# Kernel tuning notes

Measured on AMD Instinct MI355X. Metric: run time of the kernel, lower is better.

The kernel has to match this reference:

```python
import jax, jax.numpy as jnp
import numpy as np

H = 768        # hidden_size (rubert-base)
WDIM = 30      # width_embedding_dim (SpanRepresentation default)
MAXW = 10      # max_span_width
HID = 150      # PairwiseScorer hidden_dim
LN_EPS = 1e-5


def setup_inputs() -> dict:
    key = jax.random.key(0)
    ks = jax.random.split(key, 12)
    B, S, N = 4, 2048, 4096
    p = lambda i, shape: jax.random.normal(ks[i], shape, dtype=jnp.float32) * 0.02
    return {
        "sequence_output": jax.random.normal(ks[0], (B, S, H), dtype=jnp.float32),
        "span_starts": jax.random.randint(ks[1], (B, N), 0, S),
        "span_ends": jax.random.randint(ks[2], (B, N), 0, S),
        "W_start": p(3, (H, H)), "b_start": jnp.zeros((H,), jnp.float32),
        "W_end": p(4, (H, H)), "b_end": jnp.zeros((H,), jnp.float32),
        "width_emb": p(5, (MAXW + 1, WDIM)),
        "W_out": p(6, (2 * H + WDIM, H)), "b_out": jnp.zeros((H,), jnp.float32),
        "w_ment": p(7, (H,)), "b_ment": jnp.zeros((), jnp.float32),
        "W1": p(8, (4 * H, HID)), "b1": jnp.zeros((HID,), jnp.float32),
        "ln_g": jnp.ones((HID,), jnp.float32), "ln_b": jnp.zeros((HID,), jnp.float32),
        "W2": p(9, (HID,)), "b2": jnp.zeros((), jnp.float32),
        "top_k": 128,
    }


def reference(sequence_output, span_starts, span_ends,
              W_start, b_start, W_end, b_end, width_emb, W_out, b_out,
              w_ment, b_ment, W1, b1, ln_g, ln_b, W2, b2, top_k):
    # --- SpanRepresentation: gather endpoints, endpoint FFs, width embedding ---
    st = jnp.take_along_axis(sequence_output, span_starts[..., None], axis=1)  # [B,N,H]
    en = jnp.take_along_axis(sequence_output, span_ends[..., None], axis=1)    # [B,N,H]
    start_e = st @ W_start + b_start
    end_e = en @ W_end + b_end
    widths = jnp.clip(span_ends - span_starts, 0, MAXW)
    we = width_emb[widths]                                                     # [B,N,WDIM]
    span_repr = jnp.concatenate([start_e, end_e, we], axis=-1) @ W_out + b_out # [B,N,H]

    # --- MentionScorer + top-k filtering (per batch, vectorized) ---
    scores = span_repr @ w_ment + b_ment                                       # [B,N]
    mention_scores, idx = jax.lax.top_k(scores, top_k)                         # [B,K]
    repr_k = jnp.take_along_axis(span_repr, idx[..., None], axis=1)            # [B,K,H]
    f_starts = jnp.take_along_axis(span_starts, idx, axis=1)
    f_ends = jnp.take_along_axis(span_ends, idx, axis=1)

    # --- PairwiseScorer over all pairs: cat([s1,s2,s1-s2,s1*s2]) @ W1 ---
    # Split W1 rows into the four feature blocks; fold the (s1-s2) block in:
    #   z = s1@(Wa+Wc) + s2@(Wb-Wc) + (s1*s2)@Wd + b1
    Wa, Wb, Wc, Wd = W1[:H], W1[H:2*H], W1[2*H:3*H], W1[3*H:]
    u = repr_k @ (Wa + Wc)                                                     # [B,K,HID]
    v = repr_k @ (Wb - Wc)                                                     # [B,K,HID]
    pw = jnp.einsum('bih,bjh,hd->bijd', repr_k, repr_k, Wd)                    # [B,K,K,HID]
    z = u[:, :, None, :] + v[:, None, :, :] + pw + b1
    h = jax.nn.relu(z)
    mu = jnp.mean(h, axis=-1, keepdims=True)
    var = jnp.mean(jnp.square(h - mu), axis=-1, keepdims=True)
    hn = (h - mu) * jax.lax.rsqrt(var + LN_EPS) * ln_g + ln_b
    # Dropout(0.3) is identity in eval mode.
    ant = hn @ W2 + b2                                                         # [B,K,K]
    ant = jnp.tril(ant, k=-1)

    return (mention_scores, ant, f_starts, f_ends)
```

## Files before the change

### kernel.cpp

```cpp
#include <hip/hip_runtime.h>
#include <math.h>

#define H 768
#define SEQ 2048
#define NSP 4096
#define HIDD 150
#define TOPK 128
#define NPAD 160

#define OFS_ANT 512
#define OFS_FS 66048
#define OFS_FE 66560

static const size_t OFF_T     = 0ull;
static const size_t OFF_BIASP = 8448ull;
static const size_t OFF_WOV   = 14592ull;
static const size_t OFF_AV    = 16128ull;
static const size_t OFF_CV    = 16896ull;
static const size_t OFF_TW    = 17664ull;
static const size_t OFF_PD    = 17680ull;
static const size_t OFF_CAND  = 34064ull;
static const size_t OFF_FS    = 42256ull;
static const size_t OFF_FE    = 42768ull;
static const size_t OFF_WID   = 43280ull;
static const size_t OFF_UVP   = 43792ull;
static const size_t OFF_GW    = 371472ull;
static const size_t OFF_SCAL  = 371632ull;
static const size_t OFF_WF    = 371640ull;
static const size_t OFF_WCF   = 433080ull;
static const size_t OFF_WSF   = 555960ull;
static const size_t OFF_WEF   = 850872ull;
static const size_t OFF_WOF   = 1145784ull;
static const size_t OFF_SEH   = 1735608ull;
static const size_t OFF_RKH   = 2128824ull;
static const size_t OFF_RKP2  = 2325432ull;

typedef __attribute__((ext_vector_type(8))) _Float16 half8;
typedef __attribute__((ext_vector_type(4))) _Float16 half4;
typedef __attribute__((ext_vector_type(4))) float f32x4;

__global__ __launch_bounds__(256) void kA(
    const float* __restrict__ b_start, const float* __restrict__ b_end,
    const float* __restrict__ b_out, const float* __restrict__ W_out,
    const float* __restrict__ w_ment, const float* __restrict__ W1,
    const float* __restrict__ ln_g, const float* __restrict__ ln_b,
    const float* __restrict__ W2, const float* __restrict__ b2,
    const float* __restrict__ W_start, const float* __restrict__ W_end,
    float* __restrict__ biasP, float* __restrict__ WOV,
    _Float16* __restrict__ WF, _Float16* __restrict__ WCF,
    _Float16* __restrict__ WSF, _Float16* __restrict__ WEF,
    _Float16* __restrict__ WOF, float* __restrict__ GW, float* __restrict__ SCAL,
    float* __restrict__ ant) {
    const int blk = blockIdx.x, tid = threadIdx.x;
    if (blk < 24) {
        const int kc = blk / 3, jb = blk - kc * 3;
        const int j = jb * 256 + tid;
        float acc = (kc == 0) ? b_out[j] : 0.f;
        const int k0 = kc * 96;
#pragma unroll 4
        for (int k = k0; k < k0 + 96; ++k) {
            acc += b_start[k] * W_out[(size_t)k * H + j];
            acc += b_end[k]   * W_out[(size_t)(H + k) * H + j];
        }
        biasP[kc * H + j] = acc;
    } else if (blk < 408) {
        const int wid = tid >> 6, lane = tid & 63;
        const int gr = (blk - 24) * 4 + wid;
        const float* row = W_out + (size_t)gr * H;
        float s = 0.f;
#pragma unroll
        for (int q = 0; q < 12; ++q) s += row[lane + 64 * q] * w_ment[lane + 64 * q];
#pragma unroll
        for (int off = 32; off; off >>= 1) s += __shfl_down(s, off, 64);
        if (lane == 0) WOV[gr] = s;
    } else if (blk < 468) {
        const int idx = (blk - 408) * 256 + tid;
        const int nt = idx / 1536;
        const int rem = idx - nt * 1536;
        const int kt = rem >> 6, lane = rem & 63;
        const int n = nt * 16 + (lane & 15);
        const int kb = kt * 32 + (lane >> 4) * 8;
        _Float16* dst = WF + ((size_t)((kt * 10 + nt) * 64 + lane)) * 8;
#pragma unroll
        for (int e = 0; e < 8; ++e) {
            float v = (n < HIDD) ? W1[(size_t)(3 * H + kb + e) * HIDD + n] : 0.f;
            dst[e] = (_Float16)v;
        }
    } else if (blk < 588) {
        const int idx = (blk - 468) * 256 + tid;
        const int nt = idx / 1536;
        const int rem = idx - nt * 1536;
        const int kt = rem >> 6, lane = rem & 63;
        const int n = nt * 16 + (lane & 15);
        const int kb = kt * 32 + (lane >> 4) * 8;
        _Float16* dst = WCF + (size_t)idx * 8;
#pragma unroll
        for (int e = 0; e < 8; ++e) {
            const int h = kb + e;
            float v = 0.f;
            if (n < 160) {
                if (n < HIDD)
                    v = W1[(size_t)h * HIDD + n] + W1[(size_t)(2 * H + h) * HIDD + n];
            } else {
                const int d = n - 160;
                if (d < HIDD)
                    v = W1[(size_t)(H + h) * HIDD + d] - W1[(size_t)(2 * H + h) * HIDD + d];
            }
            dst[e] = (_Float16)v;
        }
    } else if (blk == 588) {
        if (tid < NPAD) GW[tid] = (tid < HIDD) ? ln_g[tid] * W2[tid] : 0.f;
        if (tid == 0) {
            float sg = 0.f, sb = 0.f;
            for (int d = 0; d < HIDD; ++d) { sg += ln_g[d] * W2[d]; sb += ln_b[d] * W2[d]; }
            SCAL[0] = sg;
            SCAL[1] = sb + b2[0];
        }
    } else if (blk < 1165) {
        const bool isS = blk < 877;
        const int idx = (blk - (isS ? 589 : 877)) * 256 + tid;
        const float* Wsrc = isS ? W_start : W_end;
        _Float16* dstb = isS ? WSF : WEF;
        const int nt = idx / 1536;
        const int rem = idx - nt * 1536;
        const int kt = rem >> 6, lane = rem & 63;
        const int n = nt * 16 + (lane & 15);
        const int kb = kt * 32 + (lane >> 4) * 8;
        _Float16* dst = dstb + (size_t)idx * 8;
#pragma unroll
        for (int e = 0; e < 8; ++e) dst[e] = (_Float16)Wsrc[(size_t)(kb + e) * H + n];
    } else if (blk < 1741) {
        const int idx = (blk - 1165) * 256 + tid;
        const int nt = idx / 3072;
        const int rem = idx - nt * 3072;
        const int kt = rem >> 6, lane = rem & 63;
        const int n = nt * 16 + (lane & 15);
        const int kb = kt * 32 + (lane >> 4) * 8;
        _Float16* dst = WOF + (size_t)idx * 8;
#pragma unroll
        for (int e = 0; e < 8; ++e) dst[e] = (_Float16)W_out[(size_t)(kb + e) * H + n];
    } else {
        const int idx = (blk - 1741) * 256 + tid;
        *(float4*)(ant + (size_t)idx * 4) = make_float4(0.f, 0.f, 0.f, 0.f);
    }
}

__global__ __launch_bounds__(256) void kB(
    const float* __restrict__ biasP, const float* __restrict__ width_emb,
    const float* __restrict__ W_out, const float* __restrict__ W_start,
    const float* __restrict__ W_end, const float* __restrict__ WOV,
    float* __restrict__ T, float* __restrict__ av, float* __restrict__ cv) {
    const int blk = blockIdx.x, tid = threadIdx.x;
    if (blk < 33) {
        const int w = blk / 3, jb = blk - w * 3;
        const int j = jb * 256 + tid;
        float acc = 0.f;
#pragma unroll
        for (int kc = 0; kc < 8; ++kc) acc += biasP[kc * H + j];
#pragma unroll
        for (int k = 0; k < 30; ++k)
            acc += width_emb[w * 30 + k] * W_out[(size_t)(2 * H + k) * H + j];
        T[w * H + j] = acc;
    } else {
        const int wid = tid >> 6, lane = tid & 63;
        const int gr = (blk - 33) * 4 + wid;
        const float* row = (gr < H) ? (W_start + (size_t)gr * H) : (W_end + (size_t)(gr - H) * H);
        const float* vec = (gr < H) ? WOV : (WOV + H);
        float s = 0.f;
#pragma unroll
        for (int q = 0; q < 12; ++q) s += row[lane + 64 * q] * vec[lane + 64 * q];
#pragma unroll
        for (int off = 32; off; off >>= 1) s += __shfl_down(s, off, 64);
        if (lane == 0) {
            if (gr < H) av[gr] = s; else cv[gr - H] = s;
        }
    }
}

__global__ void k_posdots(const float* __restrict__ seq, const float* __restrict__ av,
                          const float* __restrict__ cv, const float* __restrict__ T,
                          const float* __restrict__ w_ment, const float* __restrict__ b_ment,
                          float* __restrict__ PD, float* __restrict__ tw) {
    const int wid = threadIdx.x >> 6, lane = threadIdx.x & 63;
    if (blockIdx.x < 2048) {
        const int r = blockIdx.x * 4 + wid;
        const float4* row = (const float4*)(seq + (size_t)r * H);
        const float4* a4 = (const float4*)av;
        const float4* c4 = (const float4*)cv;
        float sa = 0.f, sc = 0.f;
#pragma unroll
        for (int q = 0; q < 3; ++q) {
            float4 x = row[lane + 64 * q];
            float4 ya = a4[lane + 64 * q], yc = c4[lane + 64 * q];
            sa += x.x * ya.x + x.y * ya.y + x.z * ya.z + x.w * ya.w;
            sc += x.x * yc.x + x.y * yc.y + x.z * yc.z + x.w * yc.w;
        }
#pragma unroll
        for (int off = 32; off; off >>= 1) {
            sa += __shfl_down(sa, off, 64);
            sc += __shfl_down(sc, off, 64);
        }
        if (lane == 0) { PD[r] = sa; PD[8192 + r] = sc; }
    } else {
        for (int w = wid; w <= 10; w += 4) {
            float s = 0.f;
#pragma unroll
            for (int q = 0; q < 12; ++q) s += T[w * H + lane + 64 * q] * w_ment[lane + 64 * q];
#pragma unroll
            for (int off = 32; off; off >>= 1) s += __shfl_down(s, off, 64);
            if (lane == 0) tw[w] = s + b_ment[0];
        }
    }
}

__global__ __launch_bounds__(256) void k_sort1(const float* __restrict__ PD,
    const int* __restrict__ starts, const int* __restrict__ ends,
    const float* __restrict__ tw, unsigned long long* __restrict__ CAND) {
    __shared__ unsigned long long keys[512];
    const int blk = blockIdx.x;
    const int b = blk >> 3, c = blk & 7;
    const int tid = threadIdx.x;
    for (int i = tid; i < 512; i += 256) {
        const int gi = c * 512 + i;
        const int r = b * NSP + gi;
        const int s = starts[r], e = ends[r];
        int w = e - s; w = w < 0 ? 0 : (w > 10 ? 10 : w);
        const float sc = PD[b * SEQ + s] + PD[8192 + b * SEQ + e] + tw[w];
        unsigned u = __float_as_uint(sc);
        u = (u & 0x80000000u) ? ~u : (u | 0x80000000u);
        keys[i] = ((unsigned long long)u << 32) | (unsigned)(0xFFFFFFFFu - (unsigned)gi);
    }
    __syncthreads();
    for (int k = 2; k <= 512; k <<= 1) {
        for (int j = k >> 1; j > 0; j >>= 1) {
            const int p = tid;
            const int i = ((p & ~(j - 1)) << 1) | (p & (j - 1));
            const int l = i | j;
            unsigned long long a = keys[i], d = keys[l];
            const bool desc = ((i & k) == 0);
            if ((a < d) == desc) { keys[i] = d; keys[l] = a; }
            __syncthreads();
        }
    }
    if (tid < 128) CAND[(size_t)(b * 8 + c) * 128 + tid] = keys[tid];
}

__global__ __launch_bounds__(256) void k_sort2(const unsigned long long* __restrict__ CAND,
    const int* __restrict__ starts, const int* __restrict__ ends,
    float* __restrict__ out, int* __restrict__ fsI, int* __restrict__ feI,
    int* __restrict__ widI) {
    __shared__ unsigned long long K[1024];
    const int b = blockIdx.x, tid = threadIdx.x;
    for (int i = tid; i < 1024; i += 256) K[i] = CAND[(size_t)b * 1024 + i];
    __syncthreads();
    for (int nl = 4; nl >= 1; nl >>= 1) {
        const int items = nl * 128;
        unsigned long long v0 = 0, v1 = 0;
        if (tid < items) {
            const int q = tid >> 7, r = tid & 127;
            unsigned long long a = K[q * 256 + r];
            unsigned long long d = K[q * 256 + 128 + (127 - r)];
            v0 = a > d ? a : d;
        }
        if (tid + 256 < items) {
            const int i = tid + 256;
            const int q = i >> 7, r = i & 127;
            unsigned long long a = K[q * 256 + r];
            unsigned long long d = K[q * 256 + 128 + (127 - r)];
            v1 = a > d ? a : d;
        }
        __syncthreads();
        if (tid < items) K[(tid >> 7) * 128 + (tid & 127)] = v0;
        if (tid + 256 < items) { const int i = tid + 256; K[(i >> 7) * 128 + (i & 127)] = v1; }
        __syncthreads();
        for (int j = 64; j; j >>= 1) {
            const int pairs = nl * 64;
            for (int i = tid; i < pairs; i += 256) {
                const int q = i >> 6, r = i & 63;
                const int lo = q * 128 + (((r & ~(j - 1)) << 1) | (r & (j - 1)));
                const int hi = lo + j;
                unsigned long long a = K[lo], d = K[hi];
                if (a < d) { K[lo] = d; K[hi] = a; }
            }
            __syncthreads();
        }
    }
    if (tid < TOPK) {
        const unsigned long long key = K[tid];
        const int widx = (int)(0xFFFFFFFFu - (unsigned)(key & 0xFFFFFFFFu));
        const unsigned hu = (unsigned)(key >> 32);
        const float sval = __uint_as_float((hu & 0x80000000u) ? (hu & 0x7FFFFFFFu) : ~hu);
        const int s = starts[b * NSP + widx], e = ends[b * NSP + widx];
        const int p = b * TOPK + tid;
        out[p] = sval;
        out[OFS_FS + p] = (float)s;
        out[OFS_FE + p] = (float)e;
        fsI[p] = b * SEQ + s;
        feI[p] = b * SEQ + e;
        int w = e - s;
        widI[p] = w < 0 ? 0 : (w > 10 ? 10 : w);
    }
}

__global__ __launch_bounds__(256) void k_gemm1(const float* __restrict__ seq,
    const int* __restrict__ fsI, const int* __restrict__ feI,
    const _Float16* __restrict__ WSF, const _Float16* __restrict__ WEF,
    _Float16* __restrict__ SEH) {
    const int mt = blockIdx.x;
    const int wave = threadIdx.x >> 6, lane = threadIdx.x & 63;
    const int g = lane >> 4;
    const int nt0 = blockIdx.y * 8 + wave * 2;
    const int gi = mt * 16 + (lane & 15);
    const int src = (mt < 32) ? fsI[gi] : feI[gi - 512];
    const float* Arow = seq + (size_t)src * H + g * 8;
    const _Float16* BF = (mt < 32) ? WSF : WEF;
    f32x4 acc0 = {0.f, 0.f, 0.f, 0.f}, acc1 = acc0;
    float4 v0 = *(const float4*)(Arow);
    float4 v1 = *(const float4*)(Arow + 4);
    half8 b0 = *(const half8*)(BF + ((size_t)(nt0 * 24) * 64 + lane) * 8);
    half8 b1 = *(const half8*)(BF + ((size_t)((nt0 + 1) * 24) * 64 + lane) * 8);
    for (int kt = 0; kt < 24; ++kt) {
        float4 nv0, nv1;
        half8 nb0, nb1;
        if (kt < 23) {
            nv0 = *(const float4*)(Arow + (kt + 1) * 32);
            nv1 = *(const float4*)(Arow + (kt + 1) * 32 + 4);
            nb0 = *(const half8*)(BF + ((size_t)(nt0 * 24 + kt + 1) * 64 + lane) * 8);
            nb1 = *(const half8*)(BF + ((size_t)((nt0 + 1) * 24 + kt + 1) * 64 + lane) * 8);
        }
        half8 a = {(_Float16)v0.x, (_Float16)v0.y, (_Float16)v0.z, (_Float16)v0.w,
                   (_Float16)v1.x, (_Float16)v1.y, (_Float16)v1.z, (_Float16)v1.w};
        acc0 = __builtin_amdgcn_mfma_f32_16x16x32_f16(a, b0, acc0, 0, 0, 0);
        acc1 = __builtin_amdgcn_mfma_f32_16x16x32_f16(a, b1, acc1, 0, 0, 0);
        if (kt < 23) { v0 = nv0; v1 = nv1; b0 = nb0; b1 = nb1; }
    }
    const int c = lane & 15, quad = lane >> 4;
#pragma unroll
    for (int r = 0; r < 4; ++r) {
        const int row = mt * 16 + quad * 4 + r;
        SEH[(size_t)row * H + nt0 * 16 + c] = (_Float16)acc0[r];
        SEH[(size_t)row * H + (nt0 + 1) * 16 + c] = (_Float16)acc1[r];
    }
}

__global__ __launch_bounds__(256) void k_gemm2(const _Float16* __restrict__ SEH,
    const _Float16* __restrict__ WOF, float* __restrict__ RKP2) {
    const int mt = blockIdx.x, kh = blockIdx.z;
    const int wave = threadIdx.x >> 6, lane = threadIdx.x & 63;
    const int nt0 = blockIdx.y * 8 + wave * 2;
    const _Float16* Arow = SEH + (size_t)(kh * 512 + mt * 16 + (lane & 15)) * H + (lane >> 4) * 8;
    const _Float16* B0 = WOF + ((size_t)(nt0 * 48 + kh * 24) * 64 + lane) * 8;
    const _Float16* B1 = WOF + ((size_t)((nt0 + 1) * 48 + kh * 24) * 64 + lane) * 8;
    f32x4 acc0 = {0.f, 0.f, 0.f, 0.f}, acc1 = acc0;
    half8 a = *(const half8*)(Arow);
    half8 b0 = *(const half8*)(B0);
    half8 b1 = *(const half8*)(B1);
    for (int kt2 = 0; kt2 < 24; ++kt2) {
        half8 na, nb0, nb1;
        if (kt2 < 23) {
            na = *(const half8*)(Arow + (kt2 + 1) * 32);
            nb0 = *(const half8*)(B0 + (size_t)(kt2 + 1) * 512);
            nb1 = *(const half8*)(B1 + (size_t)(kt2 + 1) * 512);
        }
        acc0 = __builtin_amdgcn_mfma_f32_16x16x32_f16(a, b0, acc0, 0, 0, 0);
        acc1 = __builtin_amdgcn_mfma_f32_16x16x32_f16(a, b1, acc1, 0, 0, 0);
        if (kt2 < 23) { a = na; b0 = nb0; b1 = nb1; }
    }
    const int c = lane & 15, quad = lane >> 4;
    float* dst = RKP2 + (size_t)kh * 512 * H;
#pragma unroll
    for (int r = 0; r < 4; ++r) {
        const int row = mt * 16 + quad * 4 + r;
        dst[(size_t)row * H + nt0 * 16 + c] = acc0[r];
        dst[(size_t)row * H + (nt0 + 1) * 16 + c] = acc1[r];
    }
}

__global__ void k_fin(const float* __restrict__ RKP2, const float* __restrict__ T,
                      const int* __restrict__ widI, _Float16* __restrict__ RKH) {
    const int p = blockIdx.x, tid = threadIdx.x;
    if (tid >= 192) return;
    const int w = widI[p];
    const int c0 = tid * 4;
    float4 s = *(const float4*)(T + (size_t)w * H + c0);
    float4 v0 = *(const float4*)(RKP2 + (size_t)p * H + c0);
    float4 v1 = *(const float4*)(RKP2 + (size_t)(512 + p) * H + c0);
    half4 h = {(_Float16)(s.x + v0.x + v1.x), (_Float16)(s.y + v0.y + v1.y),
               (_Float16)(s.z + v0.z + v1.z), (_Float16)(s.w + v0.w + v1.w)};
    *(half4*)(RKH + (size_t)p * H + c0) = h;
}

__global__ __launch_bounds__(256) void k_uv3(const _Float16* __restrict__ RKH,
    const _Float16* __restrict__ WCF, float* __restrict__ UVP) {
    const int t = blockIdx.x, kh = blockIdx.y;
    const int wave = threadIdx.x >> 6, lane = threadIdx.x & 63;
    const _Float16* Arow = RKH + (size_t)(t * 16 + (lane & 15)) * H + (lane >> 4) * 8 + kh * 384;
    f32x4 acc[5];
#pragma unroll
    for (int q = 0; q < 5; ++q) acc[q] = (f32x4){0.f, 0.f, 0.f, 0.f};
    half8 a = *(const half8*)(Arow);
    half8 bv[5], nbv[5];
#pragma unroll
    for (int q = 0; q < 5; ++q)
        bv[q] = *(const half8*)(WCF + ((size_t)(((wave * 5 + q) * 24 + kh * 12) * 64 + lane)) * 8);
    for (int kk = 0; kk < 12; ++kk) {
        half8 na;
        if (kk < 11) {
            const int kt = kh * 12 + kk + 1;
            na = *(const half8*)(Arow + (kk + 1) * 32);
#pragma unroll
            for (int q = 0; q < 5; ++q)
                nbv[q] = *(const half8*)(WCF + ((size_t)(((wave * 5 + q) * 24 + kt) * 64 + lane)) * 8);
        }
#pragma unroll
        for (int q = 0; q < 5; ++q)
            acc[q] = __builtin_amdgcn_mfma_f32_16x16x32_f16(a, bv[q], acc[q], 0, 0, 0);
        if (kk < 11) {
            a = na;
#pragma unroll
            for (int q = 0; q < 5; ++q) bv[q] = nbv[q];
        }
    }
    const int c = lane & 15, g = lane >> 4;
#pragma unroll
    for (int q = 0; q < 5; ++q) {
        const int n = (wave * 5 + q) * 16 + c;
#pragma unroll
        for (int r = 0; r < 4; ++r) {
            const int p = t * 16 + g * 4 + r;
            UVP[((size_t)kh * 512 + p) * 320 + n] = acc[q][r];
        }
    }
}

__global__ __launch_bounds__(256, 1) void k_pair(
    const _Float16* __restrict__ WF, const _Float16* __restrict__ RKH,
    const float* __restrict__ UVP, const float* __restrict__ b1,
    const float* __restrict__ GW, const float* __restrict__ SCAL,
    float* __restrict__ ant) {
    const int b = blockIdx.y;
    int ti = 0, rem = blockIdx.x;
    while (rem >= (ti >> 1) + 1) { rem -= (ti >> 1) + 1; ++ti; }
    const int tj = rem;
    const int wave = threadIdx.x >> 6, lane = threadIdx.x & 63;
    const int g = lane >> 4, c = lane & 15;
    const int i0 = ti * 8 + wave * 2;
    const int j0 = tj * 16;

    const _Float16* Ri0 = RKH + (size_t)(b * TOPK + i0) * H + g * 8;
    const _Float16* Ri1 = RKH + (size_t)(b * TOPK + i0 + 1) * H + g * 8;
    const _Float16* Rj  = RKH + (size_t)(b * TOPK + j0 + c) * H + g * 8;
    const _Float16* Wl  = WF + (size_t)lane * 8;

    f32x4 acc0[10], acc1[10];
#pragma unroll
    for (int nt = 0; nt < 10; ++nt) {
        acc0[nt] = (f32x4){0.f, 0.f, 0.f, 0.f};
        acc1[nt] = (f32x4){0.f, 0.f, 0.f, 0.f};
    }

    half8 bv[10], nbv[10];
    half8 rj, ri0, ri1, nrj, nri0, nri1;
#pragma unroll
    for (int nt = 0; nt < 10; ++nt) bv[nt] = *(const half8*)(Wl + (size_t)nt * 512);
    rj  = *(const half8*)(Rj);
    ri0 = *(const half8*)(Ri0);
    ri1 = *(const half8*)(Ri1);

    for (int kt = 0; kt < 24; ++kt) {
        if (kt < 23) {
            const _Float16* wsrc = Wl + (size_t)(kt + 1) * 5120;
#pragma unroll
            for (int nt = 0; nt < 10; ++nt) nbv[nt] = *(const half8*)(wsrc + (size_t)nt * 512);
            nrj  = *(const half8*)(Rj + (kt + 1) * 32);
            nri0 = *(const half8*)(Ri0 + (kt + 1) * 32);
            nri1 = *(const half8*)(Ri1 + (kt + 1) * 32);
        }
        half8 a0 = ri0 * rj;
        half8 a1 = ri1 * rj;
#pragma unroll
        for (int nt = 0; nt < 10; ++nt) {
            acc0[nt] = __builtin_amdgcn_mfma_f32_16x16x32_f16(a0, bv[nt], acc0[nt], 0, 0, 0);
            acc1[nt] = __builtin_amdgcn_mfma_f32_16x16x32_f16(a1, bv[nt], acc1[nt], 0, 0, 0);
        }
        if (kt < 23) {
#pragma unroll
            for (int nt = 0; nt < 10; ++nt) bv[nt] = nbv[nt];
            rj = nrj; ri0 = nri0; ri1 = nri1;
        }
    }

    const float Sgw = SCAL[0], C0 = SCAL[1];
    float gw10[10];
#pragma unroll
    for (int nt = 0; nt < 10; ++nt) gw10[nt] = GW[nt * 16 + c];

#pragma unroll
    for (int iw = 0; iw < 2; ++iw) {
        const int i = i0 + iw;
        const int pi = b * TOPK + i;
        float u10[10];
#pragma unroll
        for (int nt = 0; nt < 10; ++nt) {
            const int d = nt * 16 + c;
            const float ub = (d < HIDD) ? b1[d] : 0.f;
            u10[nt] = UVP[(size_t)pi * 320 + d] + UVP[(size_t)(512 + pi) * 320 + d] + ub;
        }
        const f32x4* acc = iw ? acc1 : acc0;
#pragma unroll
        for (int r = 0; r < 4; ++r) {
            const int j = j0 + g * 4 + r;
            const int pj = b * TOPK + j;
            const float* Vp0 = UVP + (size_t)pj * 320 + 160;
            const float* Vp1 = UVP + (size_t)(512 + pj) * 320 + 160;
            float s1 = 0.f, s2 = 0.f, s3 = 0.f;
#pragma unroll
            for (int nt = 0; nt < 10; ++nt) {
                const int d = nt * 16 + c;
                float z = acc[nt][r] + u10[nt] + Vp0[d] + Vp1[d];
                float h = (d < HIDD && z > 0.f) ? z : 0.f;
                s1 += h;
                s2 += h * h;
                s3 += h * gw10[nt];
            }
#pragma unroll
            for (int off = 1; off < 16; off <<= 1) {
                s1 += __shfl_xor(s1, off, 64);
                s2 += __shfl_xor(s2, off, 64);
                s3 += __shfl_xor(s3, off, 64);
            }
            const float mu = s1 * (1.f / HIDD);
            const float var = s2 * (1.f / HIDD) - mu * mu;
            const float rstd = rsqrtf(var + 1e-5f);
            const float val = rstd * (s3 - mu * Sgw) + C0;
            if (c == 0 && j < i) ant[((size_t)b * TOPK + i) * TOPK + j] = val;
        }
    }
}

extern "C" void kernel_launch(void* const* d_in, const int* in_sizes, int n_in,
                              void* d_out, int out_size, void* d_ws, size_t ws_size,
                              hipStream_t stream) {
    const float* seq      = (const float*)d_in[0];
    const int*   starts   = (const int*)d_in[1];
    const int*   ends     = (const int*)d_in[2];
    const float* W_start  = (const float*)d_in[3];
    const float* b_start  = (const float*)d_in[4];
    const float* W_end    = (const float*)d_in[5];
    const float* b_end    = (const float*)d_in[6];
    const float* width_e  = (const float*)d_in[7];
    const float* W_out    = (const float*)d_in[8];
    const float* b_out    = (const float*)d_in[9];
    const float* w_ment   = (const float*)d_in[10];
    const float* b_ment   = (const float*)d_in[11];
    const float* W1       = (const float*)d_in[12];
    const float* b1       = (const float*)d_in[13];
    const float* ln_g     = (const float*)d_in[14];
    const float* ln_b     = (const float*)d_in[15];
    const float* W2       = (const float*)d_in[16];
    const float* b2       = (const float*)d_in[17];
    float* out = (float*)d_out;
    float* ws  = (float*)d_ws;

    float* Tt    = ws + OFF_T;
    float* biasP = ws + OFF_BIASP;
    float* WOV   = ws + OFF_WOV;
    float* av    = ws + OFF_AV;
    float* cv    = ws + OFF_CV;
    float* tw    = ws + OFF_TW;
    float* PD    = ws + OFF_PD;
    unsigned long long* CANDp = (unsigned long long*)(ws + OFF_CAND);
    int*   fsI   = (int*)(ws + OFF_FS);
    int*   feI   = (int*)(ws + OFF_FE);
    int*   widI  = (int*)(ws + OFF_WID);
    float* UVPp  = ws + OFF_UVP;
    float* GWp   = ws + OFF_GW;
    float* SCALp = ws + OFF_SCAL;
    _Float16* WFp   = (_Float16*)(ws + OFF_WF);
    _Float16* WCFp  = (_Float16*)(ws + OFF_WCF);
    _Float16* WSFp  = (_Float16*)(ws + OFF_WSF);
    _Float16* WEFp  = (_Float16*)(ws + OFF_WEF);
    _Float16* WOFp  = (_Float16*)(ws + OFF_WOF);
    _Float16* SEHp  = (_Float16*)(ws + OFF_SEH);
    _Float16* RKHp  = (_Float16*)(ws + OFF_RKH);
    float* RKP2p = ws + OFF_RKP2;

    kA<<<1805, 256, 0, stream>>>(b_start, b_end, b_out, W_out, w_ment, W1,
                                 ln_g, ln_b, W2, b2, W_start, W_end,
                                 biasP, WOV, WFp, WCFp, WSFp, WEFp, WOFp, GWp, SCALp,
                                 out + OFS_ANT);
    kB<<<417, 256, 0, stream>>>(biasP, width_e, W_out, W_start, W_end, WOV, Tt, av, cv);
    k_posdots<<<2049, 256, 0, stream>>>(seq, av, cv, Tt, w_ment, b_ment, PD, tw);
    k_sort1<<<32, 256, 0, stream>>>(PD, starts, ends, tw, CANDp);
    k_sort2<<<4, 256, 0, stream>>>(CANDp, starts, ends, out, fsI, feI, widI);
    k_gemm1<<<dim3(64, 6), 256, 0, stream>>>(seq, fsI, feI, WSFp, WEFp, SEHp);
    k_gemm2<<<dim3(32, 6, 2), 256, 0, stream>>>(SEHp, WOFp, RKP2p);
    k_fin<<<512, 192, 0, stream>>>(RKP2p, Tt, widI, RKHp);
    k_uv3<<<dim3(32, 2), 256, 0, stream>>>(RKHp, WCFp, UVPp);
    k_pair<<<dim3(72, 4), 256, 0, stream>>>(WFp, RKHp, UVPp, b1, GWp, SCALp,
                                            out + OFS_ANT);
}
```

Measured before the change: 201.8 us.

## Rebalance launch graph: merge sorts, fuse fin into uv3, move weight prep

Moves the fp16 weight repacking and output zeroing out of the first kernel and into the position-dot kernel, so that independent work fills the same launch as the memory-bound dot products. It also replaces the two-stage top-k sort (32 blocks plus 4 blocks, with a global candidate buffer) with a single 1024-thread block per batch, and folds the k_fin conversion into k_uv3 through a shared-memory A tile. The goal is fewer kernel launches and less launch/serialization overhead. In exchange, the single sort kernel runs only 4 blocks, and the RKH conversion work is now spread over only 64 blocks.

```diff
diff --git a/kernel.cpp b/kernel.cpp
--- a/kernel.cpp
+++ b/kernel.cpp
@@ -19,38 +19,30 @@
 static const size_t OFF_CV    = 16896ull;
 static const size_t OFF_TW    = 17664ull;
 static const size_t OFF_PD    = 17680ull;
-static const size_t OFF_CAND  = 34064ull;
-static const size_t OFF_FS    = 42256ull;
-static const size_t OFF_FE    = 42768ull;
-static const size_t OFF_WID   = 43280ull;
-static const size_t OFF_UVP   = 43792ull;
-static const size_t OFF_GW    = 371472ull;
-static const size_t OFF_SCAL  = 371632ull;
-static const size_t OFF_WF    = 371640ull;
-static const size_t OFF_WCF   = 433080ull;
-static const size_t OFF_WSF   = 555960ull;
-static const size_t OFF_WEF   = 850872ull;
-static const size_t OFF_WOF   = 1145784ull;
-static const size_t OFF_SEH   = 1735608ull;
-static const size_t OFF_RKH   = 2128824ull;
-static const size_t OFF_RKP2  = 2325432ull;
+static const size_t OFF_FS    = 34064ull;
+static const size_t OFF_FE    = 34576ull;
+static const size_t OFF_WID   = 35088ull;
+static const size_t OFF_UVP   = 35600ull;
+static const size_t OFF_GW    = 363280ull;
+static const size_t OFF_SCAL  = 363440ull;
+static const size_t OFF_WF    = 363448ull;
+static const size_t OFF_WCF   = 424888ull;
+static const size_t OFF_WSF   = 547768ull;
+static const size_t OFF_WEF   = 842680ull;
+static const size_t OFF_WOF   = 1137592ull;
+static const size_t OFF_SEH   = 1727416ull;
+static const size_t OFF_RKH   = 2120632ull;
+static const size_t OFF_RKP2  = 2317240ull;
 
 typedef __attribute__((ext_vector_type(8))) _Float16 half8;
 typedef __attribute__((ext_vector_type(4))) _Float16 half4;
 typedef __attribute__((ext_vector_type(4))) float f32x4;
 
-__global__ __launch_bounds__(256) void kA(
+__global__ __launch_bounds__(256) void kP1(
     const float* __restrict__ b_start, const float* __restrict__ b_end,
     const float* __restrict__ b_out, const float* __restrict__ W_out,
-    const float* __restrict__ w_ment, const float* __restrict__ W1,
-    const float* __restrict__ ln_g, const float* __restrict__ ln_b,
-    const float* __restrict__ W2, const float* __restrict__ b2,
-    const float* __restrict__ W_start, const float* __restrict__ W_end,
-    float* __restrict__ biasP, float* __restrict__ WOV,
-    _Float16* __restrict__ WF, _Float16* __restrict__ WCF,
-    _Float16* __restrict__ WSF, _Float16* __restrict__ WEF,
-    _Float16* __restrict__ WOF, float* __restrict__ GW, float* __restrict__ SCAL,
-    float* __restrict__ ant) {
+    const float* __restrict__ w_ment,
+    float* __restrict__ biasP, float* __restrict__ WOV) {
     const int blk = blockIdx.x, tid = threadIdx.x;
     if (blk < 24) {
         const int kc = blk / 3, jb = blk - kc * 3;
@@ -63,7 +55,7 @@
             acc += b_end[k]   * W_out[(size_t)(H + k) * H + j];
         }
         biasP[kc * H + j] = acc;
-    } else if (blk < 408) {
+    } else {
         const int wid = tid >> 6, lane = tid & 63;
         const int gr = (blk - 24) * 4 + wid;
         const float* row = W_out + (size_t)gr * H;
@@ -73,26 +65,104 @@
 #pragma unroll
         for (int off = 32; off; off >>= 1) s += __shfl_down(s, off, 64);
         if (lane == 0) WOV[gr] = s;
-    } else if (blk < 468) {
-        const int idx = (blk - 408) * 256 + tid;
+    }
+}
+
+__global__ __launch_bounds__(256) void kP2(
+    const float* __restrict__ biasP, const float* __restrict__ width_emb,
+    const float* __restrict__ W_out, const float* __restrict__ W_start,
+    const float* __restrict__ W_end, const float* __restrict__ WOV,
+    float* __restrict__ T, float* __restrict__ av, float* __restrict__ cv) {
+    const int blk = blockIdx.x, tid = threadIdx.x;
+    if (blk < 33) {
+        const int w = blk / 3, jb = blk - w * 3;
+        const int j = jb * 256 + tid;
+        float acc = 0.f;
+#pragma unroll
+        for (int kc = 0; kc < 8; ++kc) acc += biasP[kc * H + j];
+#pragma unroll
+        for (int k = 0; k < 30; ++k)
+            acc += width_emb[w * 30 + k] * W_out[(size_t)(2 * H + k) * H + j];
+        T[w * H + j] = acc;
+    } else {
+        const int wid = tid >> 6, lane = tid & 63;
+        const int gr = (blk - 33) * 4 + wid;
+        const float* row = (gr < H) ? (W_start + (size_t)gr * H) : (W_end + (size_t)(gr - H) * H);
+        const float* vec = (gr < H) ? WOV : (WOV + H);
+        float s = 0.f;
+#pragma unroll
+        for (int q = 0; q < 12; ++q) s += row[lane + 64 * q] * vec[lane + 64 * q];
+#pragma unroll
+        for (int off = 32; off; off >>= 1) s += __shfl_down(s, off, 64);
+        if (lane == 0) {
+            if (gr < H) av[gr] = s; else cv[gr - H] = s;
+        }
+    }
+}
+
+__global__ __launch_bounds__(256) void kPost(
+    const float* __restrict__ seq, const float* __restrict__ av,
+    const float* __restrict__ cv, const float* __restrict__ T,
+    const float* __restrict__ w_ment, const float* __restrict__ b_ment,
+    const float* __restrict__ W1, const float* __restrict__ W_start,
+    const float* __restrict__ W_end, const float* __restrict__ W_out,
+    const float* __restrict__ ln_g, const float* __restrict__ ln_b,
+    const float* __restrict__ W2, const float* __restrict__ b2,
+    float* __restrict__ PD, float* __restrict__ tw,
+    _Float16* __restrict__ WF, _Float16* __restrict__ WCF,
+    _Float16* __restrict__ WSF, _Float16* __restrict__ WEF,
+    _Float16* __restrict__ WOF, float* __restrict__ GW, float* __restrict__ SCAL,
+    float* __restrict__ ant) {
+    const int blk = blockIdx.x, tid = threadIdx.x;
+    const int wid = tid >> 6, lane = tid & 63;
+    if (blk < 2048) {
+        const int r = blk * 4 + wid;
+        const float4* row = (const float4*)(seq + (size_t)r * H);
+        const float4* a4 = (const float4*)av;
+        const float4* c4 = (const float4*)cv;
+        float sa = 0.f, sc = 0.f;
+#pragma unroll
+        for (int q = 0; q < 3; ++q) {
+            float4 x = row[lane + 64 * q];
+            float4 ya = a4[lane + 64 * q], yc = c4[lane + 64 * q];
+            sa += x.x * ya.x + x.y * ya.y + x.z * ya.z + x.w * ya.w;
+            sc += x.x * yc.x + x.y * yc.y + x.z * yc.z + x.w * yc.w;
+        }
+#pragma unroll
+        for (int off = 32; off; off >>= 1) {
+            sa += __shfl_down(sa, off, 64);
+            sc += __shfl_down(sc, off, 64);
+        }
+        if (lane == 0) { PD[r] = sa; PD[8192 + r] = sc; }
+    } else if (blk == 2048) {
+        for (int w = wid; w <= 10; w += 4) {
+            float s = 0.f;
+#pragma unroll
+            for (int q = 0; q < 12; ++q) s += T[w * H + lane + 64 * q] * w_ment[lane + 64 * q];
+#pragma unroll
+            for (int off = 32; off; off >>= 1) s += __shfl_down(s, off, 64);
+            if (lane == 0) tw[w] = s + b_ment[0];
+        }
+    } else if (blk < 2109) {
+        const int idx = (blk - 2049) * 256 + tid;
         const int nt = idx / 1536;
         const int rem = idx - nt * 1536;
-        const int kt = rem >> 6, lane = rem & 63;
-        const int n = nt * 16 + (lane & 15);
-        const int kb = kt * 32 + (lane >> 4) * 8;
-        _Float16* dst = WF + ((size_t)((kt * 10 + nt) * 64 + lane)) * 8;
+        const int kt = rem >> 6, ln = rem & 63;
+        const int n = nt * 16 + (ln & 15);
+        const int kb = kt * 32 + (ln >> 4) * 8;
+        _Float16* dst = WF + ((size_t)((kt * 10 + nt) * 64 + ln)) * 8;
 #pragma unroll
         for (int e = 0; e < 8; ++e) {
             float v = (n < HIDD) ? W1[(size_t)(3 * H + kb + e) * HIDD + n] : 0.f;
             dst[e] = (_Float16)v;
         }
-    } else if (blk < 588) {
-        const int idx = (blk - 468) * 256 + tid;
+    } else if (blk < 2229) {
+        const int idx = (blk - 2109) * 256 + tid;
         const int nt = idx / 1536;
         const int rem = idx - nt * 1536;
-        const int kt = rem >> 6, lane = rem & 63;
-        const int n = nt * 16 + (lane & 15);
-        const int kb = kt * 32 + (lane >> 4) * 8;
+        const int kt = rem >> 6, ln = rem & 63;
+        const int n = nt * 16 + (ln & 15);
+        const int kb = kt * 32 + (ln >> 4) * 8;
         _Float16* dst = WCF + (size_t)idx * 8;
 #pragma unroll
         for (int e = 0; e < 8; ++e) {
@@ -108,7 +178,30 @@
             }
             dst[e] = (_Float16)v;
         }
-    } else if (blk == 588) {
+    } else if (blk < 2805) {
+        const bool isS = blk < 2517;
+        const int idx = (blk - (isS ? 2229 : 2517)) * 256 + tid;
+        const float* Wsrc = isS ? W_start : W_end;
+        _Float16* dstb = isS ? WSF : WEF;
+        const int nt = idx / 1536;
+        const int rem = idx - nt * 1536;
+        const int kt = rem >> 6, ln = rem & 63;
+        const int n = nt * 16 + (ln & 15);
+        const int kb = kt * 32 + (ln >> 4) * 8;
+        _Float16* dst = dstb + (size_t)idx * 8;
+#pragma unroll
+        for (int e = 0; e < 8; ++e) dst[e] = (_Float16)Wsrc[(size_t)(kb + e) * H + n];
+    } else if (blk < 3381) {
+        const int idx = (blk - 2805) * 256 + tid;
+        const int nt = idx / 3072;
+        const int rem = idx - nt * 3072;
+        const int kt = rem >> 6, ln = rem & 63;
+        const int n = nt * 16 + (ln & 15);
+        const int kb = kt * 32 + (ln >> 4) * 8;
+        _Float16* dst = WOF + (size_t)idx * 8;
+#pragma unroll
+        for (int e = 0; e < 8; ++e) dst[e] = (_Float16)W_out[(size_t)(kb + e) * H + n];
+    } else if (blk == 3381) {
         if (tid < NPAD) GW[tid] = (tid < HIDD) ? ln_g[tid] * W2[tid] : 0.f;
         if (tid == 0) {
             float sg = 0.f, sb = 0.f;
@@ -116,167 +209,63 @@
             SCAL[0] = sg;
             SCAL[1] = sb + b2[0];
         }
-    } else if (blk < 1165) {
-        const bool isS = blk < 877;
-        const int idx = (blk - (isS ? 589 : 877)) * 256 + tid;
-        const float* Wsrc = isS ? W_start : W_end;
-        _Float16* dstb = isS ? WSF : WEF;
-        const int nt = idx / 1536;
-        const int rem = idx - nt * 1536;
-        const int kt = rem >> 6, lane = rem & 63;
-        const int n = nt * 16 + (lane & 15);
-        const int kb = kt * 32 + (lane >> 4) * 8;
-        _Float16* dst = dstb + (size_t)idx * 8;
-#pragma unroll
-        for (int e = 0; e < 8; ++e) dst[e] = (_Float16)Wsrc[(size_t)(kb + e) * H + n];
-    } else if (blk < 1741) {
-        const int idx = (blk - 1165) * 256 + tid;
-        const int nt = idx / 3072;
-        const int rem = idx - nt * 3072;
-        const int kt = rem >> 6, lane = rem & 63;
-        const int n = nt * 16 + (lane & 15);
-        const int kb = kt * 32 + (lane >> 4) * 8;
-        _Float16* dst = WOF + (size_t)idx * 8;
-#pragma unroll
-        for (int e = 0; e < 8; ++e) dst[e] = (_Float16)W_out[(size_t)(kb + e) * H + n];
     } else {
-        const int idx = (blk - 1741) * 256 + tid;
+        const int idx = (blk - 3382) * 256 + tid;
         *(float4*)(ant + (size_t)idx * 4) = make_float4(0.f, 0.f, 0.f, 0.f);
     }
 }
 
-__global__ __launch_bounds__(256) void kB(
-    const float* __restrict__ biasP, const float* __restrict__ width_emb,
-    const float* __restrict__ W_out, const float* __restrict__ W_start,
-    const float* __restrict__ W_end, const float* __restrict__ WOV,
-    float* __restrict__ T, float* __restrict__ av, float* __restrict__ cv) {
-    const int blk = blockIdx.x, tid = threadIdx.x;
-    if (blk < 33) {
-        const int w = blk / 3, jb = blk - w * 3;
-        const int j = jb * 256 + tid;
-        float acc = 0.f;
-#pragma unroll
-        for (int kc = 0; kc < 8; ++kc) acc += biasP[kc * H + j];
-#pragma unroll
-        for (int k = 0; k < 30; ++k)
-            acc += width_emb[w * 30 + k] * W_out[(size_t)(2 * H + k) * H + j];
-        T[w * H + j] = acc;
-    } else {
-        const int wid = tid >> 6, lane = tid & 63;
-        const int gr = (blk - 33) * 4 + wid;
-        const float* row = (gr < H) ? (W_start + (size_t)gr * H) : (W_end + (size_t)(gr - H) * H);
-        const float* vec = (gr < H) ? WOV : (WOV + H);
-        float s = 0.f;
-#pragma unroll
-        for (int q = 0; q < 12; ++q) s += row[lane + 64 * q] * vec[lane + 64 * q];
-#pragma unroll
-        for (int off = 32; off; off >>= 1) s += __shfl_down(s, off, 64);
-        if (lane == 0) {
-            if (gr < H) av[gr] = s; else cv[gr - H] = s;
-        }
-    }
-}
-
-__global__ void k_posdots(const float* __restrict__ seq, const float* __restrict__ av,
-                          const float* __restrict__ cv, const float* __restrict__ T,
-                          const float* __restrict__ w_ment, const float* __restrict__ b_ment,
-                          float* __restrict__ PD, float* __restrict__ tw) {
-    const int wid = threadIdx.x >> 6, lane = threadIdx.x & 63;
-    if (blockIdx.x < 2048) {
-        const int r = blockIdx.x * 4 + wid;
-        const float4* row = (const float4*)(seq + (size_t)r * H);
-        const float4* a4 = (const float4*)av;
-        const float4* c4 = (const float4*)cv;
-        float sa = 0.f, sc = 0.f;
-#pragma unroll
-        for (int q = 0; q < 3; ++q) {
-            float4 x = row[lane + 64 * q];
-            float4 ya = a4[lane + 64 * q], yc = c4[lane + 64 * q];
-            sa += x.x * ya.x + x.y * ya.y + x.z * ya.z + x.w * ya.w;
-            sc += x.x * yc.x + x.y * yc.y + x.z * yc.z + x.w * yc.w;
-        }
-#pragma unroll
-        for (int off = 32; off; off >>= 1) {
-            sa += __shfl_down(sa, off, 64);
-            sc += __shfl_down(sc, off, 64);
-        }
-        if (lane == 0) { PD[r] = sa; PD[8192 + r] = sc; }
-    } else {
-        for (int w = wid; w <= 10; w += 4) {
-            float s = 0.f;
-#pragma unroll
-            for (int q = 0; q < 12; ++q) s += T[w * H + lane + 64 * q] * w_ment[lane + 64 * q];
-#pragma unroll
-            for (int off = 32; off; off >>= 1) s += __shfl_down(s, off, 64);
-            if (lane == 0) tw[w] = s + b_ment[0];
-        }
-    }
-}
-
-__global__ __launch_bounds__(256) void k_sort1(const float* __restrict__ PD,
+__global__ __launch_bounds__(1024) void k_sort(const float* __restrict__ PD,
     const int* __restrict__ starts, const int* __restrict__ ends,
-    const float* __restrict__ tw, unsigned long long* __restrict__ CAND) {
-    __shared__ unsigned long long keys[512];
-    const int blk = blockIdx.x;
-    const int b = blk >> 3, c = blk & 7;
-    const int tid = threadIdx.x;
-    for (int i = tid; i < 512; i += 256) {
-        const int gi = c * 512 + i;
-        const int r = b * NSP + gi;
+    const float* __restrict__ tw, float* __restrict__ out,
+    int* __restrict__ fsI, int* __restrict__ feI, int* __restrict__ widI) {
+    __shared__ unsigned long long K[4096];
+    const int b = blockIdx.x, tid = threadIdx.x;
+    for (int i = tid; i < 4096; i += 1024) {
+        const int r = b * NSP + i;
         const int s = starts[r], e = ends[r];
         int w = e - s; w = w < 0 ? 0 : (w > 10 ? 10 : w);
         const float sc = PD[b * SEQ + s] + PD[8192 + b * SEQ + e] + tw[w];
         unsigned u = __float_as_uint(sc);
         u = (u & 0x80000000u) ? ~u : (u | 0x80000000u);
-        keys[i] = ((unsigned long long)u << 32) | (unsigned)(0xFFFFFFFFu - (unsigned)gi);
+        K[i] = ((unsigned long long)u << 32) | (unsigned)(0xFFFFFFFFu - (unsigned)i);
     }
     __syncthreads();
     for (int k = 2; k <= 512; k <<= 1) {
         for (int j = k >> 1; j > 0; j >>= 1) {
-            const int p = tid;
-            const int i = ((p & ~(j - 1)) << 1) | (p & (j - 1));
-            const int l = i | j;
-            unsigned long long a = keys[i], d = keys[l];
-            const bool desc = ((i & k) == 0);
-            if ((a < d) == desc) { keys[i] = d; keys[l] = a; }
+#pragma unroll
+            for (int pp = 0; pp < 2; ++pp) {
+                const int p = tid + pp * 1024;
+                const int c = p >> 8, r = p & 255;
+                const int il = ((r & ~(j - 1)) << 1) | (r & (j - 1));
+                const int lo = c * 512 + il, hi = lo + j;
+                unsigned long long a = K[lo], d = K[hi];
+                const bool desc = ((il & k) == 0);
+                if ((a < d) == desc) { K[lo] = d; K[hi] = a; }
+            }
             __syncthreads();
         }
     }
-    if (tid < 128) CAND[(size_t)(b * 8 + c) * 128 + tid] = keys[tid];
-}
-
-__global__ __launch_bounds__(256) void k_sort2(const unsigned long long* __restrict__ CAND,
-    const int* __restrict__ starts, const int* __restrict__ ends,
-    float* __restrict__ out, int* __restrict__ fsI, int* __restrict__ feI,
-    int* __restrict__ widI) {
-    __shared__ unsigned long long K[1024];
-    const int b = blockIdx.x, tid = threadIdx.x;
-    for (int i = tid; i < 1024; i += 256) K[i] = CAND[(size_t)b * 1024 + i];
+    unsigned long long v = K[(tid >> 7) * 512 + (tid & 127)];
+    __syncthreads();
+    K[tid] = v;
     __syncthreads();
     for (int nl = 4; nl >= 1; nl >>= 1) {
         const int items = nl * 128;
-        unsigned long long v0 = 0, v1 = 0;
+        unsigned long long v0 = 0;
         if (tid < items) {
             const int q = tid >> 7, r = tid & 127;
             unsigned long long a = K[q * 256 + r];
             unsigned long long d = K[q * 256 + 128 + (127 - r)];
             v0 = a > d ? a : d;
         }
-        if (tid + 256 < items) {
-            const int i = tid + 256;
-            const int q = i >> 7, r = i & 127;
-            unsigned long long a = K[q * 256 + r];
-            unsigned long long d = K[q * 256 + 128 + (127 - r)];
-            v1 = a > d ? a : d;
-        }
         __syncthreads();
         if (tid < items) K[(tid >> 7) * 128 + (tid & 127)] = v0;
-        if (tid + 256 < items) { const int i = tid + 256; K[(i >> 7) * 128 + (i & 127)] = v1; }
         __syncthreads();
         for (int j = 64; j; j >>= 1) {
             const int pairs = nl * 64;
-            for (int i = tid; i < pairs; i += 256) {
-                const int q = i >> 6, r = i & 63;
+            if (tid < pairs) {
+                const int q = tid >> 6, r = tid & 63;
                 const int lo = q * 128 + (((r & ~(j - 1)) << 1) | (r & (j - 1)));
                 const int hi = lo + j;
                 unsigned long long a = K[lo], d = K[hi];
@@ -376,52 +365,52 @@
     }
 }
 
-__global__ void k_fin(const float* __restrict__ RKP2, const float* __restrict__ T,
-                      const int* __restrict__ widI, _Float16* __restrict__ RKH) {
-    const int p = blockIdx.x, tid = threadIdx.x;
-    if (tid >= 192) return;
-    const int w = widI[p];
-    const int c0 = tid * 4;
-    float4 s = *(const float4*)(T + (size_t)w * H + c0);
-    float4 v0 = *(const float4*)(RKP2 + (size_t)p * H + c0);
-    float4 v1 = *(const float4*)(RKP2 + (size_t)(512 + p) * H + c0);
-    half4 h = {(_Float16)(s.x + v0.x + v1.x), (_Float16)(s.y + v0.y + v1.y),
-               (_Float16)(s.z + v0.z + v1.z), (_Float16)(s.w + v0.w + v1.w)};
-    *(half4*)(RKH + (size_t)p * H + c0) = h;
-}
-
-__global__ __launch_bounds__(256) void k_uv3(const _Float16* __restrict__ RKH,
-    const _Float16* __restrict__ WCF, float* __restrict__ UVP) {
+__global__ __launch_bounds__(256) void k_uv3(const float* __restrict__ RKP2,
+    const float* __restrict__ T, const int* __restrict__ widI,
+    const _Float16* __restrict__ WCF, _Float16* __restrict__ RKH,
+    float* __restrict__ UVP) {
     const int t = blockIdx.x, kh = blockIdx.y;
-    const int wave = threadIdx.x >> 6, lane = threadIdx.x & 63;
-    const _Float16* Arow = RKH + (size_t)(t * 16 + (lane & 15)) * H + (lane >> 4) * 8 + kh * 384;
+    const int tid = threadIdx.x;
+    __shared__ _Float16 sA[16][392];
+    for (int idx = tid; idx < 16 * 96; idx += 256) {
+        const int row = idx / 96, c4 = idx - row * 96;
+        const int p = t * 16 + row;
+        const int col = kh * 384 + c4 * 4;
+        float4 s = *(const float4*)(T + (size_t)widI[p] * H + col);
+        float4 v0 = *(const float4*)(RKP2 + (size_t)p * H + col);
+        float4 v1 = *(const float4*)(RKP2 + (size_t)(512 + p) * H + col);
+        half4 h = {(_Float16)(s.x + v0.x + v1.x), (_Float16)(s.y + v0.y + v1.y),
+                   (_Float16)(s.z + v0.z + v1.z), (_Float16)(s.w + v0.w + v1.w)};
+        *(half4*)&sA[row][c4 * 4] = h;
+        *(half4*)(RKH + (size_t)p * H + col) = h;
+    }
+    __syncthreads();
+    const int wave = tid >> 6, lane = tid & 63;
+    const int m = lane & 15, g = lane >> 4;
     f32x4 acc[5];
 #pragma unroll
     for (int q = 0; q < 5; ++q) acc[q] = (f32x4){0.f, 0.f, 0.f, 0.f};
-    half8 a = *(const half8*)(Arow);
     half8 bv[5], nbv[5];
 #pragma unroll
     for (int q = 0; q < 5; ++q)
         bv[q] = *(const half8*)(WCF + ((size_t)(((wave * 5 + q) * 24 + kh * 12) * 64 + lane)) * 8);
     for (int kk = 0; kk < 12; ++kk) {
-        half8 na;
         if (kk < 11) {
             const int kt = kh * 12 + kk + 1;
-            na = *(const half8*)(Arow + (kk + 1) * 32);
 #pragma unroll
             for (int q = 0; q < 5; ++q)
                 nbv[q] = *(const half8*)(WCF + ((size_t)(((wave * 5 + q) * 24 + kt) * 64 + lane)) * 8);
         }
+        half8 a = *(const half8*)&sA[m][kk * 32 + g * 8];
 #pragma unroll
         for (int q = 0; q < 5; ++q)
             acc[q] = __builtin_amdgcn_mfma_f32_16x16x32_f16(a, bv[q], acc[q], 0, 0, 0);
         if (kk < 11) {
-            a = na;
 #pragma unroll
             for (int q = 0; q < 5; ++q) bv[q] = nbv[q];
         }
     }
-    const int c = lane & 15, g = lane >> 4;
+    const int c = lane & 15;
 #pragma unroll
     for (int q = 0; q < 5; ++q) {
         const int n = (wave * 5 + q) * 16 + c;
@@ -569,7 +558,6 @@
     float* cv    = ws + OFF_CV;
     float* tw    = ws + OFF_TW;
     float* PD    = ws + OFF_PD;
-    unsigned long long* CANDp = (unsigned long long*)(ws + OFF_CAND);
     int*   fsI   = (int*)(ws + OFF_FS);
     int*   feI   = (int*)(ws + OFF_FE);
     int*   widI  = (int*)(ws + OFF_WID);
@@ -585,18 +573,16 @@
     _Float16* RKHp  = (_Float16*)(ws + OFF_RKH);
     float* RKP2p = ws + OFF_RKP2;
 
-    kA<<<1805, 256, 0, stream>>>(b_start, b_end, b_out, W_out, w_ment, W1,
-                                 ln_g, ln_b, W2, b2, W_start, W_end,
-                                 biasP, WOV, WFp, WCFp, WSFp, WEFp, WOFp, GWp, SCALp,
-                                 out + OFS_ANT);
-    kB<<<417, 256, 0, stream>>>(biasP, width_e, W_out, W_start, W_end, WOV, Tt, av, cv);
-    k_posdots<<<2049, 256, 0, stream>>>(seq, av, cv, Tt, w_ment, b_ment, PD, tw);
-    k_sort1<<<32, 256, 0, stream>>>(PD, starts, ends, tw, CANDp);
-    k_sort2<<<4, 256, 0, stream>>>(CANDp, starts, ends, out, fsI, feI, widI);
+    kP1<<<408, 256, 0, stream>>>(b_start, b_end, b_out, W_out, w_ment, biasP, WOV);
+    kP2<<<417, 256, 0, stream>>>(biasP, width_e, W_out, W_start, W_end, WOV, Tt, av, cv);
+    kPost<<<3446, 256, 0, stream>>>(seq, av, cv, Tt, w_ment, b_ment, W1, W_start, W_end,
+                                    W_out, ln_g, ln_b, W2, b2, PD, tw,
+                                    WFp, WCFp, WSFp, WEFp, WOFp, GWp, SCALp,
+                                    out + OFS_ANT);
+    k_sort<<<4, 1024, 0, stream>>>(PD, starts, ends, tw, out, fsI, feI, widI);
     k_gemm1<<<dim3(64, 6), 256, 0, stream>>>(seq, fsI, feI, WSFp, WEFp, SEHp);
     k_gemm2<<<dim3(32, 6, 2), 256, 0, stream>>>(SEHp, WOFp, RKP2p);
-    k_fin<<<512, 192, 0, stream>>>(RKP2p, Tt, widI, RKHp);
-    k_uv3<<<dim3(32, 2), 256, 0, stream>>>(RKHp, WCFp, UVPp);
+    k_uv3<<<dim3(32, 2), 256, 0, stream>>>(RKP2p, Tt, widI, WCFp, RKHp, UVPp);
     k_pair<<<dim3(72, 4), 256, 0, stream>>>(WFp, RKHp, UVPp, b1, GWp, SCALp,
                                             out + OFS_ANT);
 }
```

Result: slower. 218.7 us (+8.4%).
